# Optimization experiments

Measured on AMD Instinct MI355X. Metric: run time of the kernel, lower is better.

## Reference

```python
import jax, jax.numpy as jnp
import numpy as np

B, N, C, H = 4, 2048, 768, 8
D = C // H          # head_size = 96
D3 = D // 3         # projected channel dim = 32


def _linear(x, W, b):
    # torch convention: W [out, in]
    return x @ W.T + b


def setup_inputs() -> dict:
    key = jax.random.key(0)
    ks = jax.random.split(key, 11)
    s = 0.02
    return {
        "x":   jax.random.normal(ks[0], (B, N, C), dtype=jnp.float32),
        "Wqk": jax.random.normal(ks[1], (C, C), dtype=jnp.float32) * s,
        "bqk": jax.random.normal(ks[2], (C,), dtype=jnp.float32) * s,
        "Wv":  jax.random.normal(ks[3], (C, C), dtype=jnp.float32) * s,
        "bv":  jax.random.normal(ks[4], (C,), dtype=jnp.float32) * s,
        "Wo":  jax.random.normal(ks[5], (C, C), dtype=jnp.float32) * s,
        "bo":  jax.random.normal(ks[6], (C,), dtype=jnp.float32) * s,
        "We":  jax.random.normal(ks[7], (D3, D), dtype=jnp.float32) * s,
        "be":  jax.random.normal(ks[8], (D3,), dtype=jnp.float32) * s,
        "Wf":  jax.random.normal(ks[9], (D3, D), dtype=jnp.float32) * s,
        "bf":  jax.random.normal(ks[10], (D3,), dtype=jnp.float32) * s,
    }


def reference(x, Wqk, bqk, Wv, bv, Wo, bo, We, be, Wf, bf):
    b, n, c = x.shape
    # q and k come from the SAME qk_linear applied twice -> identical tensors
    qk = _linear(x, Wqk, bqk).reshape(b, n, H, D)   # [B,N,H,D]
    v_ = _linear(x, Wv, bv).reshape(b, n, H, D)     # [B,N,H,D]

    q = k = qk  # [B,N,H,D] (used as bhnd via einsum)

    # Branch 1: standard softmax attention over tokens
    scale = 1.0 / jnp.sqrt(jnp.asarray(D, dtype=x.dtype))
    scores = jnp.einsum('bnhd,bmhd->bhnm', q, k) * scale   # [B,H,N,N]
    attn = jax.nn.softmax(scores, axis=-1)                  # dropout: identity (eval)
    out1 = jnp.einsum('bhnm,bmhd->bnhd', attn, v_).reshape(b, n, C)
    out1 = _linear(out1, Wo, bo)

    # Branch 2: Linformer-style projected channel attention (per token)
    k_proj = _linear(k, We, be)    # [B,N,H,D3]
    v_proj = _linear(v_, Wf, bf)   # [B,N,H,D3]
    # k_proj^T @ q over heads: [B,N,D3,D], softmax over D
    attn_sa = jax.nn.softmax(jnp.einsum('bnhe,bnhd->bned', k_proj, q), axis=-1)
    x_ca = jnp.einsum('bnhe,bned->bnhd', v_proj, attn_sa).reshape(b, n, C)
    x_ca = _linear(x_ca, Wo, bo)

    return 0.5 * (out1 + x_ca)
```

## Files before the change

### kernel.cpp

```cpp
#include <hip/hip_runtime.h>
#include <math.h>

#define BSZ 4
#define NTOK 2048
#define CDIM 768
#define HN 8
#define DH 96
#define DP 32
#define MTOT (BSZ * NTOK)

typedef short bf16x8 __attribute__((ext_vector_type(8)));
typedef float f32x4 __attribute__((ext_vector_type(4)));

__device__ __forceinline__ unsigned short f2bf(float f) {
    union { float f; unsigned u; } v; v.f = f;
    unsigned r = v.u + 0x7FFFu + ((v.u >> 16) & 1u);
    return (unsigned short)(r >> 16);
}
__device__ __forceinline__ unsigned short f2bf_trunc(float f) {
    union { float f; unsigned u; } v; v.f = f;
    return (unsigned short)(v.u >> 16);
}
__device__ __forceinline__ float bf2f(unsigned short h) {
    union { unsigned u; float f; } v; v.u = ((unsigned)h) << 16;
    return v.f;
}

__device__ __forceinline__ void async16(const unsigned short* g, unsigned short* l) {
    __builtin_amdgcn_global_load_lds(
        (const __attribute__((address_space(1))) unsigned int*)g,
        (__attribute__((address_space(3))) unsigned int*)l,
        16, 0, 0);
}

#define TE4 1572864
#define WE4 147456
#define WE24 768

__global__ __launch_bounds__(256) void prep(const float* __restrict__ x,
                                            const float* __restrict__ Wqk,
                                            const float* __restrict__ Wv,
                                            const float* __restrict__ Wo,
                                            const float* __restrict__ We,
                                            const float* __restrict__ Wf,
                                            unsigned short* __restrict__ xhi,
                                            unsigned short* __restrict__ wqv,
                                            unsigned short* __restrict__ woh,
                                            unsigned short* __restrict__ webf,
                                            unsigned short* __restrict__ wfbf)
{
    int i = blockIdx.x * 256 + threadIdx.x;
    const float* src; unsigned short* dst; int j;
    if (i < TE4)                        { j = i;                        src = x;   dst = xhi; }
    else if (i < TE4 + WE4)             { j = i - TE4;                  src = Wqk; dst = wqv; }
    else if (i < TE4 + 2 * WE4)         { j = i - TE4 - WE4;            src = Wv;  dst = wqv + (size_t)CDIM * CDIM; }
    else if (i < TE4 + 3 * WE4)         { j = i - TE4 - 2 * WE4;        src = Wo;  dst = woh; }
    else if (i < TE4 + 3 * WE4 + WE24)  { j = i - TE4 - 3 * WE4;        src = We;  dst = webf; }
    else                                { j = i - TE4 - 3 * WE4 - WE24; src = Wf;  dst = wfbf; }
    float4 f = ((const float4*)src)[j];
    ushort4 u;
    u.x = f2bf(f.x); u.y = f2bf(f.y); u.z = f2bf(f.z); u.w = f2bf(f.w);
    ((ushort4*)dst)[j] = u;
}

__global__ __launch_bounds__(256) void gemm_qv(const unsigned short* __restrict__ Ah,
                                               const unsigned short* __restrict__ wqv,
                                               const float* __restrict__ bqk,
                                               const float* __restrict__ bv,
                                               unsigned short* __restrict__ qkbf,
                                               unsigned short* __restrict__ vbf,
                                               unsigned short* __restrict__ vbft)
{
    const int K = CDIM;
    __shared__ __align__(16) unsigned short S[2][12 * 512];

    const int tid  = threadIdx.x;
    const int lane = tid & 63;
    const int w    = tid >> 6;
    const int wy   = w >> 1;
    const int wx   = w & 1;
    const int l15  = lane & 15;
    const int quad = lane >> 4;
    const int n0   = blockIdx.x * 64;
    const int m0   = blockIdx.y * 128;

    const unsigned short* gsrc[3];
    #pragma unroll
    for (int t = 0; t < 3; ++t) {
        int c = 3 * w + t;
        gsrc[t] = (c < 8)
            ? Ah  + (size_t)(m0 + c * 16 + l15) * K + quad * 8
            : wqv + (size_t)(n0 + (c - 8) * 16 + l15) * K + quad * 8;
    }

    f32x4 acc[4][2];
    #pragma unroll
    for (int rb = 0; rb < 4; ++rb)
        #pragma unroll
        for (int cb = 0; cb < 2; ++cb) acc[rb][cb] = (f32x4)0.0f;

    #pragma unroll
    for (int t = 0; t < 3; ++t)
        async16(gsrc[t], &S[0][(3 * w + t) * 512]);
    __syncthreads();

    int cur = 0;
    for (int k0 = 0; k0 < K; k0 += 32) {
        const int nxt = cur ^ 1;
        if (k0 + 32 < K) {
            #pragma unroll
            for (int t = 0; t < 3; ++t)
                async16(gsrc[t] + k0 + 32, &S[nxt][(3 * w + t) * 512]);
        }

        bf16x8 a[4], bfr[2];
        #pragma unroll
        for (int rb = 0; rb < 4; ++rb)
            a[rb] = *(const bf16x8*)&S[cur][(wy * 4 + rb) * 512 + lane * 8];
        #pragma unroll
        for (int cb = 0; cb < 2; ++cb)
            bfr[cb] = *(const bf16x8*)&S[cur][(8 + wx * 2 + cb) * 512 + lane * 8];

        #pragma unroll
        for (int rb = 0; rb < 4; ++rb)
            #pragma unroll
            for (int cb = 0; cb < 2; ++cb)
                acc[rb][cb] = __builtin_amdgcn_mfma_f32_16x16x32_bf16(a[rb], bfr[cb], acc[rb][cb], 0, 0, 0);

        __syncthreads();
        cur = nxt;
    }

    const bool isQ = (n0 < CDIM);
    #pragma unroll
    for (int rb = 0; rb < 4; ++rb)
        #pragma unroll
        for (int cb = 0; cb < 2; ++cb)
            #pragma unroll
            for (int r = 0; r < 4; ++r) {
                int row = m0 + wy * 64 + rb * 16 + quad * 4 + r;
                int colg = n0 + wx * 32 + cb * 16 + l15;
                if (isQ) {
                    float val = acc[rb][cb][r] + bqk[colg];
                    qkbf[(size_t)row * CDIM + colg] = f2bf(val);
                } else {
                    int col = colg - CDIM;
                    float val = acc[rb][cb][r] + bv[col];
                    vbf[(size_t)row * CDIM + col] = f2bf(val);
                    int b = row >> 11, tok = row & 2047;
                    int hh = col / DH, dd = col % DH;
                    vbft[(((size_t)b * HN + hh) * DH + dd) * NTOK + tok] = f2bf(val);
                }
            }
}

#define PSTR 104

__global__ __launch_bounds__(256) void proj_gemm(const unsigned short* __restrict__ qkbf,
                                                 const unsigned short* __restrict__ vbf,
                                                 const unsigned short* __restrict__ webf,
                                                 const unsigned short* __restrict__ wfbf,
                                                 const float* __restrict__ be,
                                                 const float* __restrict__ bfv,
                                                 float* __restrict__ kp,
                                                 float* __restrict__ vp)
{
    const unsigned short* Abf = blockIdx.y ? vbf : qkbf;
    const unsigned short* Wbf = blockIdx.y ? wfbf : webf;
    const float* bias         = blockIdx.y ? bfv : be;
    float* Y                  = blockIdx.y ? vp : kp;

    __shared__ __align__(16) unsigned short As[128 * PSTR];
    __shared__ __align__(16) unsigned short Bs[32 * PSTR];

    const int tid  = threadIdx.x;
    const int lane = tid & 63;
    const int w    = tid >> 6;
    const int l15  = lane & 15;
    const int quad = lane >> 4;
    const int m0   = blockIdx.x * 128;

    {
        int r = tid & 127;
        int cb = (tid >> 7) * 12;
        #pragma unroll
        for (int t = 0; t < 12; ++t) {
            int c4 = cb + t;
            if (c4 < 24)
                *(ushort4*)&As[r * PSTR + c4 * 4] =
                    *(const ushort4*)&Abf[(size_t)(m0 + r) * DH + c4 * 4];
        }
    }
    #pragma unroll
    for (int t = 0; t < 3; ++t) {
        int idx = tid + t * 256;
        if (idx < 32 * 24) {
            int r = idx / 24, c4 = idx % 24;
            *(ushort4*)&Bs[r * PSTR + c4 * 4] = *(const ushort4*)&Wbf[r * DH + c4 * 4];
        }
    }
    __syncthreads();

    f32x4 acc[2][2];
    #pragma unroll
    for (int rb = 0; rb < 2; ++rb)
        #pragma unroll
        for (int cb = 0; cb < 2; ++cb) acc[rb][cb] = (f32x4)0.0f;

    #pragma unroll
    for (int kf = 0; kf < 3; ++kf) {
        bf16x8 a0 = *(const bf16x8*)&As[(w * 32 + l15) * PSTR + kf * 32 + quad * 8];
        bf16x8 a1 = *(const bf16x8*)&As[(w * 32 + 16 + l15) * PSTR + kf * 32 + quad * 8];
        bf16x8 b0 = *(const bf16x8*)&Bs[(l15) * PSTR + kf * 32 + quad * 8];
        bf16x8 b1 = *(const bf16x8*)&Bs[(16 + l15) * PSTR + kf * 32 + quad * 8];
        acc[0][0] = __builtin_amdgcn_mfma_f32_16x16x32_bf16(a0, b0, acc[0][0], 0, 0, 0);
        acc[0][1] = __builtin_amdgcn_mfma_f32_16x16x32_bf16(a0, b1, acc[0][1], 0, 0, 0);
        acc[1][0] = __builtin_amdgcn_mfma_f32_16x16x32_bf16(a1, b0, acc[1][0], 0, 0, 0);
        acc[1][1] = __builtin_amdgcn_mfma_f32_16x16x32_bf16(a1, b1, acc[1][1], 0, 0, 0);
    }

    #pragma unroll
    for (int rb = 0; rb < 2; ++rb)
        #pragma unroll
        for (int cb = 0; cb < 2; ++cb)
            #pragma unroll
            for (int r = 0; r < 4; ++r) {
                int row = m0 + w * 32 + rb * 16 + quad * 4 + r;
                int col = cb * 16 + l15;
                Y[(size_t)row * DP + col] = acc[rb][cb][r] + bias[col];
            }
}

#define QT 128
#define KT 32
#define PST 40
#define SCL2 0.14724420f

__global__ __launch_bounds__(256) void attn_mfma(const unsigned short* __restrict__ qk_bf,
                                                 const unsigned short* __restrict__ v_bft,
                                                 unsigned short* __restrict__ chi)
{
    __shared__ __align__(16) unsigned short KfS[2][6 * 512];
    __shared__ __align__(16) unsigned short VfS[2][6 * 512];
    __shared__ __align__(16) unsigned short Ps[QT * PST];

    const int tid  = threadIdx.x;
    const int lane = tid & 63;
    const int w    = tid >> 6;
    const int l15  = lane & 15;
    const int quad = lane >> 4;

    const int bid = blockIdx.x;
    const int bh  = (bid & 7) * 4 + ((bid >> 3) & 3);
    const int qt  = bid >> 5;
    const int b   = bh >> 3;
    const int h   = bh & 7;
    const int q0  = qt * QT;

    const unsigned short* qbase = qk_bf + (size_t)b * NTOK * CDIM + h * DH;
    const unsigned short* vtb   = v_bft + (size_t)(b * HN + h) * DH * NTOK;

    bf16x8 qf[2][3];
    #pragma unroll
    for (int rb = 0; rb < 2; ++rb)
        #pragma unroll
        for (int kf = 0; kf < 3; ++kf)
            qf[rb][kf] = *(const bf16x8*)&qbase[(size_t)(q0 + w * 32 + rb * 16 + l15) * CDIM + kf * 32 + quad * 8];

    const int  kjt   = w;
    const int  vd0   = (w - 2) * 3;
    const unsigned short* kgb = qbase + (size_t)(kjt * 16 + l15) * CDIM + quad * 8;
    const unsigned short* vgb = vtb + quad * 8;

    bf16x8 ones;
    #pragma unroll
    for (int i = 0; i < 8; ++i) ones[i] = (short)0x3F80;

    f32x4 o[2][6], ls[2];
    #pragma unroll
    for (int rb = 0; rb < 2; ++rb) {
        ls[rb] = (f32x4)0.0f;
        #pragma unroll
        for (int db = 0; db < 6; ++db) o[rb][db] = (f32x4)0.0f;
    }

    if (w < 2) {
        #pragma unroll
        for (int kf = 0; kf < 3; ++kf)
            async16(kgb + kf * 32, &KfS[0][(kf * 2 + kjt) * 512]);
    } else {
        #pragma unroll
        for (int t = 0; t < 3; ++t)
            async16(vgb + (size_t)((vd0 + t) * 16 + l15) * NTOK, &VfS[0][(vd0 + t) * 512]);
    }
    __syncthreads();

    int cur = 0;
    for (int k0 = 0; k0 < NTOK; k0 += KT) {
        const int nxt = cur ^ 1;
        if (k0 + KT < NTOK) {
            if (w < 2) {
                #pragma unroll
                for (int kf = 0; kf < 3; ++kf)
                    async16(kgb + (size_t)(k0 + KT) * CDIM + kf * 32, &KfS[nxt][(kf * 2 + kjt) * 512]);
            } else {
                #pragma unroll
                for (int t = 0; t < 3; ++t)
                    async16(vgb + (size_t)((vd0 + t) * 16 + l15) * NTOK + k0 + KT, &VfS[nxt][(vd0 + t) * 512]);
            }
        }

        f32x4 s00 = (f32x4)0.0f, s01 = (f32x4)0.0f, s10 = (f32x4)0.0f, s11 = (f32x4)0.0f;
        #pragma unroll
        for (int kf = 0; kf < 3; ++kf) {
            bf16x8 k0f = *(const bf16x8*)&KfS[cur][(kf * 2 + 0) * 512 + lane * 8];
            bf16x8 k1f = *(const bf16x8*)&KfS[cur][(kf * 2 + 1) * 512 + lane * 8];
            s00 = __builtin_amdgcn_mfma_f32_16x16x32_bf16(qf[0][kf], k0f, s00, 0, 0, 0);
            s01 = __builtin_amdgcn_mfma_f32_16x16x32_bf16(qf[0][kf], k1f, s01, 0, 0, 0);
            s10 = __builtin_amdgcn_mfma_f32_16x16x32_bf16(qf[1][kf], k0f, s10, 0, 0, 0);
            s11 = __builtin_amdgcn_mfma_f32_16x16x32_bf16(qf[1][kf], k1f, s11, 0, 0, 0);
        }

        #pragma unroll
        for (int r = 0; r < 4; ++r) {
            int pr0 = w * 32 + quad * 4 + r;
            Ps[pr0 * PST + l15]      = f2bf_trunc(exp2f(s00[r] * SCL2));
            Ps[pr0 * PST + l15 + 16] = f2bf_trunc(exp2f(s01[r] * SCL2));
            int pr1 = pr0 + 16;
            Ps[pr1 * PST + l15]      = f2bf_trunc(exp2f(s10[r] * SCL2));
            Ps[pr1 * PST + l15 + 16] = f2bf_trunc(exp2f(s11[r] * SCL2));
        }

        bf16x8 pf0 = *(const bf16x8*)&Ps[(w * 32 + l15) * PST + quad * 8];
        bf16x8 pf1 = *(const bf16x8*)&Ps[(w * 32 + 16 + l15) * PST + quad * 8];
        ls[0] = __builtin_amdgcn_mfma_f32_16x16x32_bf16(pf0, ones, ls[0], 0, 0, 0);
        ls[1] = __builtin_amdgcn_mfma_f32_16x16x32_bf16(pf1, ones, ls[1], 0, 0, 0);
        #pragma unroll
        for (int db = 0; db < 6; ++db) {
            bf16x8 vf = *(const bf16x8*)&VfS[cur][db * 512 + lane * 8];
            o[0][db] = __builtin_amdgcn_mfma_f32_16x16x32_bf16(pf0, vf, o[0][db], 0, 0, 0);
            o[1][db] = __builtin_amdgcn_mfma_f32_16x16x32_bf16(pf1, vf, o[1][db], 0, 0, 0);
        }

        __syncthreads();
        cur = nxt;
    }

    #pragma unroll
    for (int rb = 0; rb < 2; ++rb)
        #pragma unroll
        for (int r = 0; r < 4; ++r) {
            float inv = 1.0f / ls[rb][r];
            int row = w * 32 + rb * 16 + quad * 4 + r;
            size_t base = ((size_t)b * NTOK + q0 + row) * CDIM + h * DH;
            #pragma unroll
            for (int db = 0; db < 6; ++db)
                chi[base + db * 16 + l15] = f2bf(o[rb][db][r] * inv);
        }
}

#define SFS 97

__global__ __launch_bounds__(256) void branch2_v2(const unsigned short* __restrict__ qkbf,
                                                  const float* __restrict__ kpG,
                                                  const float* __restrict__ vpG,
                                                  unsigned short* __restrict__ chi)
{
    __shared__ float qrowS[CDIM];
    __shared__ float SfS[DP * SFS];
    __shared__ float kpS[HN * DP];
    __shared__ float vpS[HN * DP];
    __shared__ float ps[DP][8];
    __shared__ float invs[DP];

    const int tid = threadIdx.x;
    const size_t tok = blockIdx.x;

    if (tid < 192) {
        ushort4 u = *(const ushort4*)&qkbf[tok * CDIM + tid * 4];
        float4 f;
        f.x = bf2f(u.x); f.y = bf2f(u.y); f.z = bf2f(u.z); f.w = bf2f(u.w);
        *(float4*)&qrowS[tid * 4] = f;
    } else {
        int t = tid - 192;
        ((float4*)kpS)[t] = ((const float4*)(kpG + tok * (HN * DP)))[t];
        ((float4*)vpS)[t] = ((const float4*)(vpG + tok * (HN * DP)))[t];
    }
    __syncthreads();

    #pragma unroll
    for (int t = 0; t < 12; ++t) {
        int idx = tid + t * 256;
        int e = idx / DH, d = idx % DH;
        float s = 0.0f;
        #pragma unroll
        for (int h = 0; h < HN; ++h) s += kpS[h * DP + e] * qrowS[h * DH + d];
        SfS[e * SFS + d] = exp2f(s * 1.44269504f);
    }
    __syncthreads();

    {
        int e = tid >> 3, g = tid & 7;
        float s = 0.0f;
        #pragma unroll
        for (int j = 0; j < 12; ++j) s += SfS[e * SFS + g * 12 + j];
        ps[e][g] = s;
    }
    __syncthreads();
    if (tid < DP) {
        float s = 0.0f;
        #pragma unroll
        for (int g = 0; g < 8; ++g) s += ps[tid][g];
        invs[tid] = 1.0f / s;
    }
    __syncthreads();
    {
        int h = tid >> 5, e = tid & 31;
        vpS[h * DP + e] *= invs[e];
    }
    __syncthreads();

    #pragma unroll
    for (int t = 0; t < 3; ++t) {
        int c = tid + t * 256;
        int h = c / DH, d = c % DH;
        float s = 0.0f;
        #pragma unroll 8
        for (int e = 0; e < DP; ++e) s += vpS[h * DP + e] * SfS[e * SFS + d];
        size_t idx = tok * CDIM + c;
        chi[idx] = f2bf(bf2f(chi[idx]) + s);
    }
}

__global__ __launch_bounds__(256) void gemm_out(const unsigned short* __restrict__ Ah,
                                                const unsigned short* __restrict__ Bh,
                                                const float* __restrict__ bias,
                                                float* __restrict__ Yf)
{
    const int N = CDIM, K = CDIM;
    __shared__ __align__(16) unsigned short S[2][12 * 512];

    const int tid  = threadIdx.x;
    const int lane = tid & 63;
    const int w    = tid >> 6;
    const int wy   = w >> 1;
    const int wx   = w & 1;
    const int l15  = lane & 15;
    const int quad = lane >> 4;
    const int n0   = blockIdx.x * 64;
    const int m0   = blockIdx.y * 128;

    const unsigned short* gsrc[3];
    #pragma unroll
    for (int t = 0; t < 3; ++t) {
        int c = 3 * w + t;
        gsrc[t] = (c < 8)
            ? Ah + (size_t)(m0 + c * 16 + l15) * K + quad * 8
            : Bh + (size_t)(n0 + (c - 8) * 16 + l15) * K + quad * 8;
    }

    f32x4 acc[4][2];
    #pragma unroll
    for (int rb = 0; rb < 4; ++rb)
        #pragma unroll
        for (int cb = 0; cb < 2; ++cb) acc[rb][cb] = (f32x4)0.0f;

    #pragma unroll
    for (int t = 0; t < 3; ++t)
        async16(gsrc[t], &S[0][(3 * w + t) * 512]);
    __syncthreads();

    int cur = 0;
    for (int k0 = 0; k0 < K; k0 += 32) {
        const int nxt = cur ^ 1;
        if (k0 + 32 < K) {
            #pragma unroll
            for (int t = 0; t < 3; ++t)
                async16(gsrc[t] + k0 + 32, &S[nxt][(3 * w + t) * 512]);
        }

        bf16x8 a[4], bfr[2];
        #pragma unroll
        for (int rb = 0; rb < 4; ++rb)
            a[rb] = *(const bf16x8*)&S[cur][(wy * 4 + rb) * 512 + lane * 8];
        #pragma unroll
        for (int cb = 0; cb < 2; ++cb)
            bfr[cb] = *(const bf16x8*)&S[cur][(8 + wx * 2 + cb) * 512 + lane * 8];

        #pragma unroll
        for (int rb = 0; rb < 4; ++rb)
            #pragma unroll
            for (int cb = 0; cb < 2; ++cb)
                acc[rb][cb] = __builtin_amdgcn_mfma_f32_16x16x32_bf16(a[rb], bfr[cb], acc[rb][cb], 0, 0, 0);

        __syncthreads();
        cur = nxt;
    }

    #pragma unroll
    for (int rb = 0; rb < 4; ++rb)
        #pragma unroll
        for (int cb = 0; cb < 2; ++cb)
            #pragma unroll
            for (int r = 0; r < 4; ++r) {
                int row = m0 + wy * 64 + rb * 16 + quad * 4 + r;
                int col = n0 + wx * 32 + cb * 16 + l15;
                Yf[(size_t)row * N + col] = 0.5f * acc[rb][cb][r] + bias[col];
            }
}

extern "C" void kernel_launch(void* const* d_in, const int* in_sizes, int n_in,
                              void* d_out, int out_size, void* d_ws, size_t ws_size,
                              hipStream_t stream)
{
    (void)in_sizes; (void)n_in; (void)out_size; (void)ws_size;
    const float* x   = (const float*)d_in[0];
    const float* Wqk = (const float*)d_in[1];
    const float* bqk = (const float*)d_in[2];
    const float* Wv  = (const float*)d_in[3];
    const float* bv  = (const float*)d_in[4];
    const float* Wo  = (const float*)d_in[5];
    const float* bo  = (const float*)d_in[6];
    const float* We  = (const float*)d_in[7];
    const float* be  = (const float*)d_in[8];
    const float* Wf  = (const float*)d_in[9];
    const float* bfv = (const float*)d_in[10];
    float* out = (float*)d_out;

    const size_t TE  = (size_t)MTOT * CDIM;
    const size_t WE  = (size_t)CDIM * CDIM;
    const size_t WE2 = (size_t)DP * DH;
    const size_t PE  = (size_t)MTOT * HN * DP;

    char* p = (char*)d_ws;
    unsigned short* xhi  = (unsigned short*)p;   p += TE * 2;
    unsigned short* qkbf = (unsigned short*)p;   p += TE * 2;
    unsigned short* vbf  = (unsigned short*)p;   p += TE * 2;
    unsigned short* vbft = (unsigned short*)p;   p += TE * 2;
    unsigned short* chi  = (unsigned short*)p;   p += TE * 2;
    unsigned short* wqv  = (unsigned short*)p;   p += 2 * WE * 2;
    unsigned short* woh  = (unsigned short*)p;   p += WE * 2;
    unsigned short* webf = (unsigned short*)p;   p += WE2 * 2;
    unsigned short* wfbf = (unsigned short*)p;   p += WE2 * 2;
    float* kp            = (float*)p;            p += PE * 4;
    float* vp            = (float*)p;            p += PE * 4;

    const int prep_items = TE4 + 3 * WE4 + 2 * WE24;
    prep<<<dim3((prep_items + 255) / 256), 256, 0, stream>>>(
        x, Wqk, Wv, Wo, We, Wf, xhi, wqv, woh, webf, wfbf);

    gemm_qv<<<dim3(2 * CDIM / 64, MTOT / 128), 256, 0, stream>>>(
        xhi, wqv, bqk, bv, qkbf, vbf, vbft);

    proj_gemm<<<dim3(MTOT * HN / 128, 2), 256, 0, stream>>>(
        qkbf, vbf, webf, wfbf, be, bfv, kp, vp);

    attn_mfma<<<dim3((NTOK / QT) * BSZ * HN), 256, 0, stream>>>(qkbf, vbft, chi);

    branch2_v2<<<dim3(MTOT), 256, 0, stream>>>(qkbf, kp, vp, chi);

    gemm_out<<<dim3(CDIM / 64, MTOT / 128), 256, 0, stream>>>(chi, woh, bo, out);
}
```

Baseline: 342.4 us.

## Replace LDS-staged GEMMs with per-wave register-prefetched tiles and XCD-aware block mapping

Both projection GEMMs stop staging tiles through shared memory with block-wide barriers. Each wave now owns its own output tile (64x64 for qv, 32x64 for out) and loads MFMA fragments straight from global memory into registers, double-buffered one k-step ahead. Block IDs are remapped so that each XCD works on a contiguous range of rows, to improve L2 locality. This removes LDS traffic and syncthreads, but loses operand sharing across waves in a block, which raises global/L2 load volume and register pressure.

```diff
diff --git a/kernel.cpp b/kernel.cpp
--- a/kernel.cpp
+++ b/kernel.cpp
@@ -72,74 +72,68 @@
                                                unsigned short* __restrict__ vbft)
 {
     const int K = CDIM;
-    __shared__ __align__(16) unsigned short S[2][12 * 512];
-
     const int tid  = threadIdx.x;
     const int lane = tid & 63;
     const int w    = tid >> 6;
-    const int wy   = w >> 1;
-    const int wx   = w & 1;
     const int l15  = lane & 15;
     const int quad = lane >> 4;
-    const int n0   = blockIdx.x * 64;
-    const int m0   = blockIdx.y * 128;
-
-    const unsigned short* gsrc[3];
-    #pragma unroll
-    for (int t = 0; t < 3; ++t) {
-        int c = 3 * w + t;
-        gsrc[t] = (c < 8)
-            ? Ah  + (size_t)(m0 + c * 16 + l15) * K + quad * 8
-            : wqv + (size_t)(n0 + (c - 8) * 16 + l15) * K + quad * 8;
-    }
-
-    f32x4 acc[4][2];
+
+    const int bid  = blockIdx.x;
+    const int xcd  = bid & 7;
+    const int idx2 = (bid >> 3) * 4 + w;
+    const int m_local = idx2 / 24;
+    const int n_idx   = idx2 % 24;
+    const int m0 = (xcd * 16 + m_local) * 64;
+    const int n0 = n_idx * 64;
+
+    const unsigned short* aA[4];
+    const unsigned short* aB[4];
     #pragma unroll
     for (int rb = 0; rb < 4; ++rb)
-        #pragma unroll
-        for (int cb = 0; cb < 2; ++cb) acc[rb][cb] = (f32x4)0.0f;
-
-    #pragma unroll
-    for (int t = 0; t < 3; ++t)
-        async16(gsrc[t], &S[0][(3 * w + t) * 512]);
-    __syncthreads();
-
-    int cur = 0;
-    for (int k0 = 0; k0 < K; k0 += 32) {
-        const int nxt = cur ^ 1;
-        if (k0 + 32 < K) {
-            #pragma unroll
-            for (int t = 0; t < 3; ++t)
-                async16(gsrc[t] + k0 + 32, &S[nxt][(3 * w + t) * 512]);
-        }
-
-        bf16x8 a[4], bfr[2];
-        #pragma unroll
-        for (int rb = 0; rb < 4; ++rb)
-            a[rb] = *(const bf16x8*)&S[cur][(wy * 4 + rb) * 512 + lane * 8];
-        #pragma unroll
-        for (int cb = 0; cb < 2; ++cb)
-            bfr[cb] = *(const bf16x8*)&S[cur][(8 + wx * 2 + cb) * 512 + lane * 8];
-
-        #pragma unroll
-        for (int rb = 0; rb < 4; ++rb)
-            #pragma unroll
-            for (int cb = 0; cb < 2; ++cb)
-                acc[rb][cb] = __builtin_amdgcn_mfma_f32_16x16x32_bf16(a[rb], bfr[cb], acc[rb][cb], 0, 0, 0);
-
-        __syncthreads();
-        cur = nxt;
-    }
-
-    const bool isQ = (n0 < CDIM);
+        aA[rb] = Ah + (size_t)(m0 + rb * 16 + l15) * K + quad * 8;
+    #pragma unroll
+    for (int cb = 0; cb < 4; ++cb)
+        aB[cb] = wqv + (size_t)(n0 + cb * 16 + l15) * K + quad * 8;
+
+    f32x4 acc[4][4];
     #pragma unroll
     for (int rb = 0; rb < 4; ++rb)
         #pragma unroll
-        for (int cb = 0; cb < 2; ++cb)
+        for (int cb = 0; cb < 4; ++cb) acc[rb][cb] = (f32x4)0.0f;
+
+    bf16x8 af[2][4], bb[2][4];
+    #pragma unroll
+    for (int rb = 0; rb < 4; ++rb) af[0][rb] = *(const bf16x8*)aA[rb];
+    #pragma unroll
+    for (int cb = 0; cb < 4; ++cb) bb[0][cb] = *(const bf16x8*)aB[cb];
+
+    for (int k0 = 0; k0 < K; k0 += 64) {
+        #pragma unroll
+        for (int kk = 0; kk < 2; ++kk) {
+            const int cur = kk, nxt = kk ^ 1;
+            int kn = k0 + kk * 32 + 32;
+            if (kn >= K) kn = 0;
+            #pragma unroll
+            for (int rb = 0; rb < 4; ++rb) af[nxt][rb] = *(const bf16x8*)(aA[rb] + kn);
+            #pragma unroll
+            for (int cb = 0; cb < 4; ++cb) bb[nxt][cb] = *(const bf16x8*)(aB[cb] + kn);
+            #pragma unroll
+            for (int rb = 0; rb < 4; ++rb)
+                #pragma unroll
+                for (int cb = 0; cb < 4; ++cb)
+                    acc[rb][cb] = __builtin_amdgcn_mfma_f32_16x16x32_bf16(af[cur][rb], bb[cur][cb], acc[rb][cb], 0, 0, 0);
+        }
+    }
+
+    const bool isQ = (n_idx < 12);
+    #pragma unroll
+    for (int rb = 0; rb < 4; ++rb)
+        #pragma unroll
+        for (int cb = 0; cb < 4; ++cb)
             #pragma unroll
             for (int r = 0; r < 4; ++r) {
-                int row = m0 + wy * 64 + rb * 16 + quad * 4 + r;
-                int colg = n0 + wx * 32 + cb * 16 + l15;
+                int row = m0 + rb * 16 + quad * 4 + r;
+                int colg = n0 + cb * 16 + l15;
                 if (isQ) {
                     float val = acc[rb][cb][r] + bqk[colg];
                     qkbf[(size_t)row * CDIM + colg] = f2bf(val);
@@ -437,75 +431,69 @@
                                                 const float* __restrict__ bias,
                                                 float* __restrict__ Yf)
 {
-    const int N = CDIM, K = CDIM;
-    __shared__ __align__(16) unsigned short S[2][12 * 512];
-
+    const int K = CDIM;
     const int tid  = threadIdx.x;
     const int lane = tid & 63;
     const int w    = tid >> 6;
-    const int wy   = w >> 1;
-    const int wx   = w & 1;
     const int l15  = lane & 15;
     const int quad = lane >> 4;
-    const int n0   = blockIdx.x * 64;
-    const int m0   = blockIdx.y * 128;
-
-    const unsigned short* gsrc[3];
-    #pragma unroll
-    for (int t = 0; t < 3; ++t) {
-        int c = 3 * w + t;
-        gsrc[t] = (c < 8)
-            ? Ah + (size_t)(m0 + c * 16 + l15) * K + quad * 8
-            : Bh + (size_t)(n0 + (c - 8) * 16 + l15) * K + quad * 8;
-    }
-
-    f32x4 acc[4][2];
-    #pragma unroll
-    for (int rb = 0; rb < 4; ++rb)
-        #pragma unroll
-        for (int cb = 0; cb < 2; ++cb) acc[rb][cb] = (f32x4)0.0f;
-
-    #pragma unroll
-    for (int t = 0; t < 3; ++t)
-        async16(gsrc[t], &S[0][(3 * w + t) * 512]);
-    __syncthreads();
-
-    int cur = 0;
-    for (int k0 = 0; k0 < K; k0 += 32) {
-        const int nxt = cur ^ 1;
-        if (k0 + 32 < K) {
-            #pragma unroll
-            for (int t = 0; t < 3; ++t)
-                async16(gsrc[t] + k0 + 32, &S[nxt][(3 * w + t) * 512]);
-        }
-
-        bf16x8 a[4], bfr[2];
-        #pragma unroll
-        for (int rb = 0; rb < 4; ++rb)
-            a[rb] = *(const bf16x8*)&S[cur][(wy * 4 + rb) * 512 + lane * 8];
-        #pragma unroll
-        for (int cb = 0; cb < 2; ++cb)
-            bfr[cb] = *(const bf16x8*)&S[cur][(8 + wx * 2 + cb) * 512 + lane * 8];
-
-        #pragma unroll
-        for (int rb = 0; rb < 4; ++rb)
-            #pragma unroll
-            for (int cb = 0; cb < 2; ++cb)
-                acc[rb][cb] = __builtin_amdgcn_mfma_f32_16x16x32_bf16(a[rb], bfr[cb], acc[rb][cb], 0, 0, 0);
-
-        __syncthreads();
-        cur = nxt;
-    }
-
-    #pragma unroll
-    for (int rb = 0; rb < 4; ++rb)
-        #pragma unroll
-        for (int cb = 0; cb < 2; ++cb)
+
+    const int bid  = blockIdx.x;
+    const int xcd  = bid & 7;
+    const int idx2 = (bid >> 3) * 4 + w;
+    const int m_local = idx2 / 12;
+    const int n_idx   = idx2 % 12;
+    const int m0 = (xcd * 32 + m_local) * 32;
+    const int n0 = n_idx * 64;
+
+    const unsigned short* aA[2];
+    const unsigned short* aB[4];
+    #pragma unroll
+    for (int rb = 0; rb < 2; ++rb)
+        aA[rb] = Ah + (size_t)(m0 + rb * 16 + l15) * K + quad * 8;
+    #pragma unroll
+    for (int cb = 0; cb < 4; ++cb)
+        aB[cb] = Bh + (size_t)(n0 + cb * 16 + l15) * K + quad * 8;
+
+    f32x4 acc[2][4];
+    #pragma unroll
+    for (int rb = 0; rb < 2; ++rb)
+        #pragma unroll
+        for (int cb = 0; cb < 4; ++cb) acc[rb][cb] = (f32x4)0.0f;
+
+    bf16x8 af[2][2], bb[2][4];
+    #pragma unroll
+    for (int rb = 0; rb < 2; ++rb) af[0][rb] = *(const bf16x8*)aA[rb];
+    #pragma unroll
+    for (int cb = 0; cb < 4; ++cb) bb[0][cb] = *(const bf16x8*)aB[cb];
+
+    for (int k0 = 0; k0 < K; k0 += 64) {
+        #pragma unroll
+        for (int kk = 0; kk < 2; ++kk) {
+            const int cur = kk, nxt = kk ^ 1;
+            int kn = k0 + kk * 32 + 32;
+            if (kn >= K) kn = 0;
+            #pragma unroll
+            for (int rb = 0; rb < 2; ++rb) af[nxt][rb] = *(const bf16x8*)(aA[rb] + kn);
+            #pragma unroll
+            for (int cb = 0; cb < 4; ++cb) bb[nxt][cb] = *(const bf16x8*)(aB[cb] + kn);
+            #pragma unroll
+            for (int rb = 0; rb < 2; ++rb)
+                #pragma unroll
+                for (int cb = 0; cb < 4; ++cb)
+                    acc[rb][cb] = __builtin_amdgcn_mfma_f32_16x16x32_bf16(af[cur][rb], bb[cur][cb], acc[rb][cb], 0, 0, 0);
+        }
+    }
+
+    #pragma unroll
+    for (int rb = 0; rb < 2; ++rb)
+        #pragma unroll
+        for (int cb = 0; cb < 4; ++cb)
             #pragma unroll
             for (int r = 0; r < 4; ++r) {
-                int row = m0 + wy * 64 + rb * 16 + quad * 4 + r;
-                int col = n0 + wx * 32 + cb * 16 + l15;
-                Yf[(size_t)row * N + col] = 0.5f * acc[rb][cb][r] + bias[col];
+                int row = m0 + rb * 16 + quad * 4 + r;
+                int col = n0 + cb * 16 + l15;
+                Yf[(size_t)row * CDIM + col] = 0.5f * acc[rb][cb][r] + bias[col];
             }
 }
 
@@ -549,7 +537,7 @@
     prep<<<dim3((prep_items + 255) / 256), 256, 0, stream>>>(
         x, Wqk, Wv, Wo, We, Wf, xhi, wqv, woh, webf, wfbf);
 
-    gemm_qv<<<dim3(2 * CDIM / 64, MTOT / 128), 256, 0, stream>>>(
+    gemm_qv<<<dim3(768), 256, 0, stream>>>(
         xhi, wqv, bqk, bv, qkbf, vbf, vbft);
 
     proj_gemm<<<dim3(MTOT * HN / 128, 2), 256, 0, stream>>>(
@@ -559,5 +547,5 @@
 
     branch2_v2<<<dim3(MTOT), 256, 0, stream>>>(qkbf, kp, vp, chi);
 
-    gemm_out<<<dim3(CDIM / 64, MTOT / 128), 256, 0, stream>>>(chi, woh, bo, out);
-}
+    gemm_out<<<dim3(768), 256, 0, stream>>>(chi, woh, bo, out);
+}
```

After: 400.5 us. 17.0% more time.

## Enlarge GEMM tiles to 128x128 with swizzled LDS and single buffering

Applied to the files above, without the earlier changes.

Both projection GEMMs (QV and output) move from 128x64 to 128x128 output tiles, giving each wave a 4x4 block of MFMA accumulators for more reuse per LDS load. The LDS layout gains an XOR swizzle on 16-byte chunks to avoid bank conflicts. Double buffering is dropped in favour of a load, sync, compute, sync loop, with launch bounds asking for three blocks per CU to hide latency. Costs: fewer blocks in the grid, more accumulator registers, and loads no longer overlapped with MFMA inside a block.

```diff
diff --git a/kernel.cpp b/kernel.cpp
--- a/kernel.cpp
+++ b/kernel.cpp
@@ -63,16 +63,17 @@
     ((ushort4*)dst)[j] = u;
 }
 
-__global__ __launch_bounds__(256) void gemm_qv(const unsigned short* __restrict__ Ah,
-                                               const unsigned short* __restrict__ wqv,
-                                               const float* __restrict__ bqk,
-                                               const float* __restrict__ bv,
-                                               unsigned short* __restrict__ qkbf,
-                                               unsigned short* __restrict__ vbf,
-                                               unsigned short* __restrict__ vbft)
+__global__ __launch_bounds__(256, 3) void gemm_qv(const unsigned short* __restrict__ Ah,
+                                                  const unsigned short* __restrict__ wqv,
+                                                  const float* __restrict__ bqk,
+                                                  const float* __restrict__ bv,
+                                                  unsigned short* __restrict__ qkbf,
+                                                  unsigned short* __restrict__ vbf,
+                                                  unsigned short* __restrict__ vbft)
 {
     const int K = CDIM;
-    __shared__ __align__(16) unsigned short S[2][12 * 512];
+    __shared__ __align__(16) unsigned short As[8 * 512];
+    __shared__ __align__(16) unsigned short Bs[8 * 512];
 
     const int tid  = threadIdx.x;
     const int lane = tid & 63;
@@ -81,65 +82,61 @@
     const int wx   = w & 1;
     const int l15  = lane & 15;
     const int quad = lane >> 4;
-    const int n0   = blockIdx.x * 64;
+    const int n0   = blockIdx.x * 128;
     const int m0   = blockIdx.y * 128;
 
-    const unsigned short* gsrc[3];
-    #pragma unroll
-    for (int t = 0; t < 3; ++t) {
-        int c = 3 * w + t;
-        gsrc[t] = (c < 8)
-            ? Ah  + (size_t)(m0 + c * 16 + l15) * K + quad * 8
-            : wqv + (size_t)(n0 + (c - 8) * 16 + l15) * K + quad * 8;
-    }
-
-    f32x4 acc[4][2];
+    const int srow   = lane >> 2;
+    const int schunk = (lane & 3) ^ ((lane >> 3) & 3);
+    const unsigned short* agp[2];
+    const unsigned short* bgp[2];
+    #pragma unroll
+    for (int t = 0; t < 2; ++t) {
+        int g = w * 2 + t;
+        agp[t] = Ah  + (size_t)(m0 + g * 16 + srow) * K + schunk * 8;
+        bgp[t] = wqv + (size_t)(n0 + g * 16 + srow) * K + schunk * 8;
+    }
+
+    const int roff = l15 * 32 + (quad ^ ((l15 >> 1) & 3)) * 8;
+
+    f32x4 acc[4][4];
     #pragma unroll
     for (int rb = 0; rb < 4; ++rb)
         #pragma unroll
-        for (int cb = 0; cb < 2; ++cb) acc[rb][cb] = (f32x4)0.0f;
-
-    #pragma unroll
-    for (int t = 0; t < 3; ++t)
-        async16(gsrc[t], &S[0][(3 * w + t) * 512]);
-    __syncthreads();
-
-    int cur = 0;
+        for (int cb = 0; cb < 4; ++cb) acc[rb][cb] = (f32x4)0.0f;
+
     for (int k0 = 0; k0 < K; k0 += 32) {
-        const int nxt = cur ^ 1;
-        if (k0 + 32 < K) {
-            #pragma unroll
-            for (int t = 0; t < 3; ++t)
-                async16(gsrc[t] + k0 + 32, &S[nxt][(3 * w + t) * 512]);
-        }
-
-        bf16x8 a[4], bfr[2];
+        #pragma unroll
+        for (int t = 0; t < 2; ++t) {
+            async16(agp[t] + k0, &As[(w * 2 + t) * 512]);
+            async16(bgp[t] + k0, &Bs[(w * 2 + t) * 512]);
+        }
+        __syncthreads();
+
+        bf16x8 a[4], bfr[4];
         #pragma unroll
         for (int rb = 0; rb < 4; ++rb)
-            a[rb] = *(const bf16x8*)&S[cur][(wy * 4 + rb) * 512 + lane * 8];
-        #pragma unroll
-        for (int cb = 0; cb < 2; ++cb)
-            bfr[cb] = *(const bf16x8*)&S[cur][(8 + wx * 2 + cb) * 512 + lane * 8];
+            a[rb] = *(const bf16x8*)&As[(wy * 4 + rb) * 512 + roff];
+        #pragma unroll
+        for (int cb = 0; cb < 4; ++cb)
+            bfr[cb] = *(const bf16x8*)&Bs[(wx * 4 + cb) * 512 + roff];
 
         #pragma unroll
         for (int rb = 0; rb < 4; ++rb)
             #pragma unroll
-            for (int cb = 0; cb < 2; ++cb)
+            for (int cb = 0; cb < 4; ++cb)
                 acc[rb][cb] = __builtin_amdgcn_mfma_f32_16x16x32_bf16(a[rb], bfr[cb], acc[rb][cb], 0, 0, 0);
-
         __syncthreads();
-        cur = nxt;
     }
 
     const bool isQ = (n0 < CDIM);
     #pragma unroll
     for (int rb = 0; rb < 4; ++rb)
         #pragma unroll
-        for (int cb = 0; cb < 2; ++cb)
+        for (int cb = 0; cb < 4; ++cb)
             #pragma unroll
             for (int r = 0; r < 4; ++r) {
                 int row = m0 + wy * 64 + rb * 16 + quad * 4 + r;
-                int colg = n0 + wx * 32 + cb * 16 + l15;
+                int colg = n0 + wx * 64 + cb * 16 + l15;
                 if (isQ) {
                     float val = acc[rb][cb][r] + bqk[colg];
                     qkbf[(size_t)row * CDIM + colg] = f2bf(val);
@@ -151,6 +148,79 @@
                     int hh = col / DH, dd = col % DH;
                     vbft[(((size_t)b * HN + hh) * DH + dd) * NTOK + tok] = f2bf(val);
                 }
+            }
+}
+
+__global__ __launch_bounds__(256, 3) void gemm_out(const unsigned short* __restrict__ Ah,
+                                                   const unsigned short* __restrict__ Bh,
+                                                   const float* __restrict__ bias,
+                                                   float* __restrict__ Yf)
+{
+    const int K = CDIM;
+    __shared__ __align__(16) unsigned short As[8 * 512];
+    __shared__ __align__(16) unsigned short Bs[8 * 512];
+
+    const int tid  = threadIdx.x;
+    const int lane = tid & 63;
+    const int w    = tid >> 6;
+    const int wy   = w >> 1;
+    const int wx   = w & 1;
+    const int l15  = lane & 15;
+    const int quad = lane >> 4;
+    const int n0   = blockIdx.x * 128;
+    const int m0   = blockIdx.y * 128;
+
+    const int srow   = lane >> 2;
+    const int schunk = (lane & 3) ^ ((lane >> 3) & 3);
+    const unsigned short* agp[2];
+    const unsigned short* bgp[2];
+    #pragma unroll
+    for (int t = 0; t < 2; ++t) {
+        int g = w * 2 + t;
+        agp[t] = Ah + (size_t)(m0 + g * 16 + srow) * K + schunk * 8;
+        bgp[t] = Bh + (size_t)(n0 + g * 16 + srow) * K + schunk * 8;
+    }
+    const int roff = l15 * 32 + (quad ^ ((l15 >> 1) & 3)) * 8;
+
+    f32x4 acc[4][4];
+    #pragma unroll
+    for (int rb = 0; rb < 4; ++rb)
+        #pragma unroll
+        for (int cb = 0; cb < 4; ++cb) acc[rb][cb] = (f32x4)0.0f;
+
+    for (int k0 = 0; k0 < K; k0 += 32) {
+        #pragma unroll
+        for (int t = 0; t < 2; ++t) {
+            async16(agp[t] + k0, &As[(w * 2 + t) * 512]);
+            async16(bgp[t] + k0, &Bs[(w * 2 + t) * 512]);
+        }
+        __syncthreads();
+
+        bf16x8 a[4], bfr[4];
+        #pragma unroll
+        for (int rb = 0; rb < 4; ++rb)
+            a[rb] = *(const bf16x8*)&As[(wy * 4 + rb) * 512 + roff];
+        #pragma unroll
+        for (int cb = 0; cb < 4; ++cb)
+            bfr[cb] = *(const bf16x8*)&Bs[(wx * 4 + cb) * 512 + roff];
+
+        #pragma unroll
+        for (int rb = 0; rb < 4; ++rb)
+            #pragma unroll
+            for (int cb = 0; cb < 4; ++cb)
+                acc[rb][cb] = __builtin_amdgcn_mfma_f32_16x16x32_bf16(a[rb], bfr[cb], acc[rb][cb], 0, 0, 0);
+        __syncthreads();
+    }
+
+    #pragma unroll
+    for (int rb = 0; rb < 4; ++rb)
+        #pragma unroll
+        for (int cb = 0; cb < 4; ++cb)
+            #pragma unroll
+            for (int r = 0; r < 4; ++r) {
+                int row = m0 + wy * 64 + rb * 16 + quad * 4 + r;
+                int col = n0 + wx * 64 + cb * 16 + l15;
+                Yf[(size_t)row * CDIM + col] = 0.5f * acc[rb][cb][r] + bias[col];
             }
 }
 
@@ -432,83 +502,6 @@
     }
 }
 
-__global__ __launch_bounds__(256) void gemm_out(const unsigned short* __restrict__ Ah,
-                                                const unsigned short* __restrict__ Bh,
-                                                const float* __restrict__ bias,
-                                                float* __restrict__ Yf)
-{
-    const int N = CDIM, K = CDIM;
-    __shared__ __align__(16) unsigned short S[2][12 * 512];
-
-    const int tid  = threadIdx.x;
-    const int lane = tid & 63;
-    const int w    = tid >> 6;
-    const int wy   = w >> 1;
-    const int wx   = w & 1;
-    const int l15  = lane & 15;
-    const int quad = lane >> 4;
-    const int n0   = blockIdx.x * 64;
-    const int m0   = blockIdx.y * 128;
-
-    const unsigned short* gsrc[3];
-    #pragma unroll
-    for (int t = 0; t < 3; ++t) {
-        int c = 3 * w + t;
-        gsrc[t] = (c < 8)
-            ? Ah + (size_t)(m0 + c * 16 + l15) * K + quad * 8
-            : Bh + (size_t)(n0 + (c - 8) * 16 + l15) * K + quad * 8;
-    }
-
-    f32x4 acc[4][2];
-    #pragma unroll
-    for (int rb = 0; rb < 4; ++rb)
-        #pragma unroll
-        for (int cb = 0; cb < 2; ++cb) acc[rb][cb] = (f32x4)0.0f;
-
-    #pragma unroll
-    for (int t = 0; t < 3; ++t)
-        async16(gsrc[t], &S[0][(3 * w + t) * 512]);
-    __syncthreads();
-
-    int cur = 0;
-    for (int k0 = 0; k0 < K; k0 += 32) {
-        const int nxt = cur ^ 1;
-        if (k0 + 32 < K) {
-            #pragma unroll
-            for (int t = 0; t < 3; ++t)
-                async16(gsrc[t] + k0 + 32, &S[nxt][(3 * w + t) * 512]);
-        }
-
-        bf16x8 a[4], bfr[2];
-        #pragma unroll
-        for (int rb = 0; rb < 4; ++rb)
-            a[rb] = *(const bf16x8*)&S[cur][(wy * 4 + rb) * 512 + lane * 8];
-        #pragma unroll
-        for (int cb = 0; cb < 2; ++cb)
-            bfr[cb] = *(const bf16x8*)&S[cur][(8 + wx * 2 + cb) * 512 + lane * 8];
-
-        #pragma unroll
-        for (int rb = 0; rb < 4; ++rb)
-            #pragma unroll
-            for (int cb = 0; cb < 2; ++cb)
-                acc[rb][cb] = __builtin_amdgcn_mfma_f32_16x16x32_bf16(a[rb], bfr[cb], acc[rb][cb], 0, 0, 0);
-
-        __syncthreads();
-        cur = nxt;
-    }
-
-    #pragma unroll
-    for (int rb = 0; rb < 4; ++rb)
-        #pragma unroll
-        for (int cb = 0; cb < 2; ++cb)
-            #pragma unroll
-            for (int r = 0; r < 4; ++r) {
-                int row = m0 + wy * 64 + rb * 16 + quad * 4 + r;
-                int col = n0 + wx * 32 + cb * 16 + l15;
-                Yf[(size_t)row * N + col] = 0.5f * acc[rb][cb][r] + bias[col];
-            }
-}
-
 extern "C" void kernel_launch(void* const* d_in, const int* in_sizes, int n_in,
                               void* d_out, int out_size, void* d_ws, size_t ws_size,
                               hipStream_t stream)
@@ -549,7 +542,7 @@
     prep<<<dim3((prep_items + 255) / 256), 256, 0, stream>>>(
         x, Wqk, Wv, Wo, We, Wf, xhi, wqv, woh, webf, wfbf);
 
-    gemm_qv<<<dim3(2 * CDIM / 64, MTOT / 128), 256, 0, stream>>>(
+    gemm_qv<<<dim3(2 * CDIM / 128, MTOT / 128), 256, 0, stream>>>(
         xhi, wqv, bqk, bv, qkbf, vbf, vbft);
 
     proj_gemm<<<dim3(MTOT * HN / 128, 2), 256, 0, stream>>>(
@@ -559,5 +552,5 @@
 
     branch2_v2<<<dim3(MTOT), 256, 0, stream>>>(qkbf, kp, vp, chi);
 
-    gemm_out<<<dim3(CDIM / 64, MTOT / 128), 256, 0, stream>>>(chi, woh, bo, out);
-}
+    gemm_out<<<dim3(CDIM / 128, MTOT / 128), 256, 0, stream>>>(chi, woh, bo, out);
+}
```

Result: faster. 299.4 us (-12.6%).
